# Kernel optimization log

Hardware: AMD Instinct MI355X
Metric: run time of the kernel (lower is better)

Reference implementation:

```python
import jax, jax.numpy as jnp
import numpy as np

B, N, D = 4, 1024, 512
H, Dv, Dq = 8, 64, 64
NUM_BUCKETS = 64
LN_EPS = 1e-5


def setup_inputs() -> dict:
    key = jax.random.key(0)
    ks = jax.random.split(key, 10)
    x = jax.random.normal(ks[0], (B, N, D), dtype=jnp.float32)
    ts = jnp.sort(jax.random.randint(ks[1], (B, N), 0, 1_000_000), axis=1).astype(jnp.int64)
    cm = jnp.triu(jnp.ones((N, N), dtype=bool), k=1)  # causal: mask j > i
    pm = jnp.zeros((B, N), dtype=bool)                # no padding
    uvqk = 0.02 * jax.random.normal(ks[2], (D, 2 * H * Dv + 2 * H * Dq), dtype=jnp.float32)
    lim = float(np.sqrt(6.0 / (H * Dv + D)))
    o_w = jax.random.uniform(ks[3], (H * Dv, D), minval=-lim, maxval=lim, dtype=jnp.float32)
    o_b = jnp.zeros((D,), dtype=jnp.float32)
    ln_x_w = jnp.ones((D,), jnp.float32); ln_x_b = jnp.zeros((D,), jnp.float32)
    ln_a_w = jnp.ones((H * Dv,), jnp.float32); ln_a_b = jnp.zeros((H * Dv,), jnp.float32)
    ts_w = 0.02 * jax.random.normal(ks[4], (NUM_BUCKETS + 1,), dtype=jnp.float32)
    pos_w = 0.02 * jax.random.normal(ks[5], (2 * N - 1,), dtype=jnp.float32)
    return {"x": x, "ts": ts, "cm": cm, "pm": pm, "uvqk": uvqk, "o_w": o_w, "o_b": o_b,
            "ln_x_w": ln_x_w, "ln_x_b": ln_x_b, "ln_a_w": ln_a_w, "ln_a_b": ln_a_b,
            "ts_w": ts_w, "pos_w": pos_w}


def _layernorm(x, w, b):
    m = jnp.mean(x, axis=-1, keepdims=True)
    v = jnp.mean(jnp.square(x - m), axis=-1, keepdims=True)
    return (x - m) / jnp.sqrt(v + LN_EPS) * w + b


def _rel_bias(ts, ts_w, pos_w):
    # positional part: pb[i, j] = pos_w[j - i + N - 1], shape [N, N]
    idx = jnp.arange(N)
    pb = pos_w[idx[None, :] - idx[:, None] + N - 1]
    # bucketed time part
    ext = jnp.concatenate([ts, ts[:, N - 1:N]], axis=1)           # [B, N+1]
    diff = ext[:, 1:, None] - ext[:, None, :-1]                   # [B, N, N]
    logd = jnp.log(jnp.maximum(jnp.abs(diff), 1).astype(jnp.float32))
    bk = jnp.clip((logd / 0.301).astype(jnp.int32), 0, NUM_BUCKETS)
    return pb[None] + ts_w[bk]                                    # [B, N, N]


def reference(x, ts, cm, pm, uvqk, o_w, o_b, ln_x_w, ln_x_b, ln_a_w, ln_a_b, ts_w, pos_w):
    nx = _layernorm(x, ln_x_w, ln_x_b)                            # [B, N, D]
    out = jax.nn.silu(jnp.einsum('bnd,de->bne', nx, uvqk))        # [B, N, 2HDv+2HDq]
    u, v, q, k = jnp.split(out, [H * Dv, 2 * H * Dv, 2 * H * Dv + H * Dq], axis=-1)
    q = q.reshape(B, N, H, Dq)
    k = k.reshape(B, N, H, Dq)
    v = v.reshape(B, N, H, Dv)
    qk = jnp.einsum('bihd,bjhd->bhij', q, k) + _rel_bias(ts, ts_w, pos_w)[:, None]
    qk = jax.nn.silu(qk) / N
    qk = jnp.where(cm[None, None], 0.0, qk)          # causal mask
    qk = jnp.where(pm[:, None, None, :], 0.0, qk)    # padding mask on keys
    ao = jnp.einsum('bhij,bjhd->bihd', qk, v).reshape(B, N, H * Dv)
    ao = _layernorm(ao, ln_a_w, ln_a_b)
    u = u.reshape(B, N, H * Dv)
    y = (u * ao) @ o_w + o_b + x
    return jnp.where(pm[:, :, None], 0.0, y)
```

## Files before the change

kernel.cpp:

```cpp
#include <hip/hip_runtime.h>


typedef __attribute__((ext_vector_type(8))) short short8;
typedef __attribute__((ext_vector_type(4))) short bf4;
typedef __attribute__((ext_vector_type(4))) float floatx4;

#define MFMA_BF16 __builtin_amdgcn_mfma_f32_16x16x32_bf16

static __device__ __forceinline__ short f2bf(float f) {
  unsigned u = __builtin_bit_cast(unsigned, f);
  u = (u + 0x7fffu + ((u >> 16) & 1u)) >> 16;
  return (short)u;
}
static __device__ __forceinline__ float bf2f(short s) {
  unsigned u = ((unsigned)(unsigned short)s) << 16;
  return __builtin_bit_cast(float, u);
}
static __device__ __forceinline__ float silu_f(float x) {
  return x / (1.f + __expf(-x));
}
static __device__ __forceinline__ void gl_lds16(const void* g, void* l) {
  __builtin_amdgcn_global_load_lds(
      (const __attribute__((address_space(1))) unsigned int*)g,
      (__attribute__((address_space(3))) unsigned int*)l, 16, 0, 0);
}

__global__ __launch_bounds__(256) void cvt_t_kernel(const float* __restrict__ src,
                                                    short* __restrict__ dst,
                                                    int R, int C) {
  __shared__ float tile[32][33];
  const int t = threadIdx.x;
  const int bc = blockIdx.x * 32, br = blockIdx.y * 32;
  const int c = t & 31, r0 = t >> 5;
#pragma unroll
  for (int p = 0; p < 4; ++p) {
    int r = r0 + p * 8;
    tile[r][c] = src[(size_t)(br + r) * C + bc + c];
  }
  __syncthreads();
#pragma unroll
  for (int p = 0; p < 4; ++p) {
    int r = r0 + p * 8;
    dst[(size_t)(bc + r) * R + br + c] = f2bf(tile[c][r]);
  }
}

__global__ __launch_bounds__(256) void ln_x_kernel(const float* __restrict__ x,
                                                   const float* __restrict__ w_,
                                                   const float* __restrict__ b_,
                                                   short* __restrict__ out) {
  const int lane = threadIdx.x & 63;
  const int row = (blockIdx.x << 2) + (threadIdx.x >> 6);
  const int c0 = lane * 8;
  const float* xr = x + (size_t)row * 512;
  float v[8];
  *(float4*)&v[0] = *(const float4*)(xr + c0);
  *(float4*)&v[4] = *(const float4*)(xr + c0 + 4);
  float s = 0.f, sq = 0.f;
#pragma unroll
  for (int e = 0; e < 8; ++e) { s += v[e]; sq += v[e] * v[e]; }
#pragma unroll
  for (int off = 32; off > 0; off >>= 1) {
    s += __shfl_xor(s, off);
    sq += __shfl_xor(sq, off);
  }
  float m = s * (1.f / 512.f);
  float var = sq * (1.f / 512.f) - m * m;
  float rinv = rsqrtf(var + 1e-5f);
  float wv[8], bv[8];
  *(float4*)&wv[0] = *(const float4*)(w_ + c0);
  *(float4*)&wv[4] = *(const float4*)(w_ + c0 + 4);
  *(float4*)&bv[0] = *(const float4*)(b_ + c0);
  *(float4*)&bv[4] = *(const float4*)(b_ + c0 + 4);
  short8 o;
#pragma unroll
  for (int e = 0; e < 8; ++e) o[e] = f2bf((v[e] - m) * rinv * wv[e] + bv[e]);
  *(short8*)(out + (size_t)row * 512 + c0) = o;
}

__global__ __launch_bounds__(256) void bias_kernel(const int* __restrict__ ts,
                                                   const float* __restrict__ ts_w,
                                                   const float* __restrict__ pos_w,
                                                   short* __restrict__ bias) {
  const int b = blockIdx.x >> 10, i = blockIdx.x & 1023;
  int ie = i + 1; if (ie > 1023) ie = 1023;
  const int tse = ts[(b << 10) + ie];
  const int j0 = threadIdx.x * 4;
  int4 tj = *(const int4*)&ts[(b << 10) + j0];
  const int* tjp = (const int*)&tj;
  bf4 o;
#pragma unroll
  for (int e = 0; e < 4; ++e) {
    int dt = tse - tjp[e];
    float ad = fabsf((float)dt);
    if (ad < 1.f) ad = 1.f;
    int bkt = (int)(__logf(ad) * (1.f / 0.301f));
    if (bkt > 64) bkt = 64;
    o[e] = f2bf(pos_w[j0 + e - i + 1023] + ts_w[bkt]);
  }
  *(bf4*)&bias[((size_t)blockIdx.x << 10) + j0] = o;
}

__global__ __launch_bounds__(256) void gemm1_kernel(
    const short* __restrict__ A, const short* __restrict__ Bt,
    short* __restrict__ u_buf, short* __restrict__ vt_buf,
    short* __restrict__ q_buf, short* __restrict__ k_buf) {
  __shared__ __align__(16) short As[128 * 32];
  __shared__ __align__(16) short Bs[128 * 32];
  const int t = threadIdx.x;
  const int lane = t & 63, w = t >> 6;
  const int quad = lane >> 4, l15 = lane & 15;
  const int m0 = blockIdx.x * 128, n0 = blockIdx.y * 128;
  const int wm = (w & 1) * 64, wn = (w >> 1) * 64;
  const int lr = lane >> 2, lc = (lane & 3) * 8;
  floatx4 acc[4][4];
#pragma unroll
  for (int i = 0; i < 4; ++i)
#pragma unroll
    for (int j = 0; j < 4; ++j) acc[i][j] = (floatx4){0.f, 0.f, 0.f, 0.f};

  for (int k0 = 0; k0 < 512; k0 += 32) {
    __syncthreads();
#pragma unroll
    for (int p = 0; p < 2; ++p) {
      int ra = w * 32 + p * 16;
      gl_lds16(&A[(size_t)(m0 + ra + lr) * 512 + k0 + lc], &As[ra * 32]);
      gl_lds16(&Bt[(size_t)(n0 + ra + lr) * 512 + k0 + lc], &Bs[ra * 32]);
    }
    __syncthreads();
    short8 af[4], bfr[4];
#pragma unroll
    for (int mi = 0; mi < 4; ++mi) af[mi] = *(const short8*)&As[(wm + mi * 16 + l15) * 32 + quad * 8];
#pragma unroll
    for (int ni = 0; ni < 4; ++ni) bfr[ni] = *(const short8*)&Bs[(wn + ni * 16 + l15) * 32 + quad * 8];
#pragma unroll
    for (int mi = 0; mi < 4; ++mi)
#pragma unroll
      for (int ni = 0; ni < 4; ++ni)
        acc[mi][ni] = MFMA_BF16(af[mi], bfr[ni], acc[mi][ni], 0, 0, 0);
  }
  const int seg = n0 >> 9, cbase = n0 & 511;
  if (seg == 0) {
#pragma unroll
    for (int mi = 0; mi < 4; ++mi)
#pragma unroll
      for (int ni = 0; ni < 4; ++ni)
#pragma unroll
        for (int r = 0; r < 4; ++r) {
          int row = m0 + wm + mi * 16 + quad * 4 + r;
          int c = cbase + wn + ni * 16 + l15;
          u_buf[(size_t)row * 512 + c] = f2bf(silu_f(acc[mi][ni][r]));
        }
  } else if (seg == 1) {
#pragma unroll
    for (int mi = 0; mi < 4; ++mi)
#pragma unroll
      for (int ni = 0; ni < 4; ++ni) {
        int c = cbase + wn + ni * 16 + l15;
        int h = c >> 6, d = c & 63;
        int row0 = m0 + wm + mi * 16 + quad * 4;
        int b_ = row0 >> 10, nb = row0 & 1023;
        bf4 sv;
#pragma unroll
        for (int r = 0; r < 4; ++r) sv[r] = f2bf(silu_f(acc[mi][ni][r]));
        *(bf4*)&vt_buf[(((size_t)(b_ * 8 + h) * 64 + d) << 10) + nb] = sv;
      }
  } else {
    short* dst = (seg == 2) ? q_buf : k_buf;
#pragma unroll
    for (int mi = 0; mi < 4; ++mi)
#pragma unroll
      for (int ni = 0; ni < 4; ++ni)
#pragma unroll
        for (int r = 0; r < 4; ++r) {
          int row = m0 + wm + mi * 16 + quad * 4 + r;
          int c = cbase + wn + ni * 16 + l15;
          int b_ = row >> 10, nseq = row & 1023;
          size_t idx = ((((size_t)(b_ * 8 + (c >> 6))) << 10) + nseq) * 64 + (c & 63);
          dst[idx] = f2bf(silu_f(acc[mi][ni][r]));
        }
  }
}

__global__ __launch_bounds__(256) void attn_kernel(
    const short* __restrict__ q_buf, const short* __restrict__ k_buf,
    const short* __restrict__ vt_buf, const short* __restrict__ bias_buf,
    short* __restrict__ ao_part) {
  __shared__ __align__(16) short q_s[64][72];
  __shared__ __align__(16) short k_s[64][72];
  __shared__ __align__(16) short vt_s[64][72];
  __shared__ __align__(16) short p_s[64][72];
  __shared__ __align__(16) short bias_s[64][72];

  const int t = threadIdx.x;
  const int lane = t & 63, w = t >> 6;
  const int quad = lane >> 4, l15 = lane & 15;
  const int bh = blockIdx.x, pair = blockIdx.y, jh = blockIdx.z;
  const int b = bh >> 3, h = bh & 7;
  const short* qh = q_buf + (size_t)bh * 65536;
  const short* kh = k_buf + (size_t)bh * 65536;
  const short* vth = vt_buf + (size_t)bh * 65536;
  const int sr = t >> 2, sc = (t & 3) * 16;

#pragma unroll
  for (int half = 0; half < 2; ++half) {
    const int it = half ? (15 - pair) : pair;
    const int i0 = it * 64;
    __syncthreads();
    *(float4*)&q_s[sr][sc] = *(const float4*)&qh[(size_t)(i0 + sr) * 64 + sc];
    *(float4*)&q_s[sr][sc + 8] = *(const float4*)&qh[(size_t)(i0 + sr) * 64 + sc + 8];
    floatx4 ao0 = {0.f, 0.f, 0.f, 0.f}, ao1 = ao0, ao2 = ao0, ao3 = ao0;
    for (int jt = jh; jt <= it; jt += 2) {
      const int j0 = jt * 64;
      __syncthreads();
      *(float4*)&k_s[sr][sc] = *(const float4*)&kh[(size_t)(j0 + sr) * 64 + sc];
      *(float4*)&k_s[sr][sc + 8] = *(const float4*)&kh[(size_t)(j0 + sr) * 64 + sc + 8];
      *(float4*)&vt_s[sr][sc] = *(const float4*)&vth[(size_t)sr * 1024 + j0 + sc];
      *(float4*)&vt_s[sr][sc + 8] = *(const float4*)&vth[(size_t)sr * 1024 + j0 + sc + 8];
      const size_t brow = ((size_t)(b * 1024 + i0 + sr) << 10) + j0 + sc;
      *(float4*)&bias_s[sr][sc] = *(const float4*)&bias_buf[brow];
      *(float4*)&bias_s[sr][sc + 8] = *(const float4*)&bias_buf[brow + 8];
      __syncthreads();
      floatx4 s0 = {0.f, 0.f, 0.f, 0.f}, s1 = s0, s2 = s0, s3 = s0;
#pragma unroll
      for (int kk = 0; kk < 64; kk += 32) {
        short8 aq = *(const short8*)&q_s[w * 16 + l15][kk + quad * 8];
        s0 = MFMA_BF16(aq, *(const short8*)&k_s[0 + l15][kk + quad * 8], s0, 0, 0, 0);
        s1 = MFMA_BF16(aq, *(const short8*)&k_s[16 + l15][kk + quad * 8], s1, 0, 0, 0);
        s2 = MFMA_BF16(aq, *(const short8*)&k_s[32 + l15][kk + quad * 8], s2, 0, 0, 0);
        s3 = MFMA_BF16(aq, *(const short8*)&k_s[48 + l15][kk + quad * 8], s3, 0, 0, 0);
      }
      const bool diag = (jt == it);
      floatx4 sv[4] = {s0, s1, s2, s3};
#pragma unroll
      for (int ni = 0; ni < 4; ++ni) {
        int j_loc = ni * 16 + l15;
#pragma unroll
        for (int r2 = 0; r2 < 4; ++r2) {
          int i_loc = w * 16 + quad * 4 + r2;
          float xx = sv[ni][r2] + bf2f(bias_s[i_loc][j_loc]);
          float pv = silu_f(xx) * (1.f / 1024.f);
          if (diag && j_loc > i_loc) pv = 0.f;
          p_s[i_loc][j_loc] = f2bf(pv);
        }
      }
#pragma unroll
      for (int kk = 0; kk < 64; kk += 32) {
        short8 ap = *(const short8*)&p_s[w * 16 + l15][kk + quad * 8];
        ao0 = MFMA_BF16(ap, *(const short8*)&vt_s[0 + l15][kk + quad * 8], ao0, 0, 0, 0);
        ao1 = MFMA_BF16(ap, *(const short8*)&vt_s[16 + l15][kk + quad * 8], ao1, 0, 0, 0);
        ao2 = MFMA_BF16(ap, *(const short8*)&vt_s[32 + l15][kk + quad * 8], ao2, 0, 0, 0);
        ao3 = MFMA_BF16(ap, *(const short8*)&vt_s[48 + l15][kk + quad * 8], ao3, 0, 0, 0);
      }
    }
    floatx4 aov[4] = {ao0, ao1, ao2, ao3};
    short* aod = ao_part + (size_t)jh * 2097152;
#pragma unroll
    for (int ni = 0; ni < 4; ++ni)
#pragma unroll
      for (int r2 = 0; r2 < 4; ++r2) {
        int gi = i0 + w * 16 + quad * 4 + r2;
        int d = ni * 16 + l15;
        aod[((size_t)(b * 1024 + gi)) * 512 + h * 64 + d] = f2bf(aov[ni][r2]);
      }
  }
}

__global__ __launch_bounds__(256) void ln_mul_kernel(
    const short* __restrict__ ao_part, const short* __restrict__ u,
    const float* __restrict__ w_, const float* __restrict__ b_,
    short* __restrict__ g) {
  const int lane = threadIdx.x & 63;
  const int row = (blockIdx.x << 2) + (threadIdx.x >> 6);
  const int c0 = lane * 8;
  short8 a0 = *(const short8*)(ao_part + (size_t)row * 512 + c0);
  short8 a1 = *(const short8*)(ao_part + 2097152 + (size_t)row * 512 + c0);
  float v[8];
#pragma unroll
  for (int e = 0; e < 8; ++e) v[e] = bf2f(a0[e]) + bf2f(a1[e]);
  float s = 0.f, sq = 0.f;
#pragma unroll
  for (int e = 0; e < 8; ++e) { s += v[e]; sq += v[e] * v[e]; }
#pragma unroll
  for (int off = 32; off > 0; off >>= 1) {
    s += __shfl_xor(s, off);
    sq += __shfl_xor(sq, off);
  }
  float m = s * (1.f / 512.f);
  float var = sq * (1.f / 512.f) - m * m;
  float rinv = rsqrtf(var + 1e-5f);
  float wv[8], bv[8];
  *(float4*)&wv[0] = *(const float4*)(w_ + c0);
  *(float4*)&wv[4] = *(const float4*)(w_ + c0 + 4);
  *(float4*)&bv[0] = *(const float4*)(b_ + c0);
  *(float4*)&bv[4] = *(const float4*)(b_ + c0 + 4);
  short8 uv = *(const short8*)(u + (size_t)row * 512 + c0);
  short8 o;
#pragma unroll
  for (int e = 0; e < 8; ++e)
    o[e] = f2bf(bf2f(uv[e]) * ((v[e] - m) * rinv * wv[e] + bv[e]));
  *(short8*)(g + (size_t)row * 512 + c0) = o;
}

__global__ __launch_bounds__(256) void gemm2_kernel(
    const short* __restrict__ G, const short* __restrict__ Wt,
    const float* __restrict__ o_b, const float* __restrict__ x,
    float* __restrict__ out) {
  __shared__ __align__(16) short As[64 * 32];
  __shared__ __align__(16) short Bs[128 * 32];
  const int t = threadIdx.x;
  const int lane = t & 63, w = t >> 6;
  const int quad = lane >> 4, l15 = lane & 15;
  const int m0 = blockIdx.x * 64, n0 = blockIdx.y * 128;
  const int wn = w * 32;
  const int lr = lane >> 2, lc = (lane & 3) * 8;
  floatx4 acc[4][2];
#pragma unroll
  for (int i = 0; i < 4; ++i)
#pragma unroll
    for (int j = 0; j < 2; ++j) acc[i][j] = (floatx4){0.f, 0.f, 0.f, 0.f};

  for (int k0 = 0; k0 < 512; k0 += 32) {
    __syncthreads();
    {
      int ra = w * 16;
      gl_lds16(&G[(size_t)(m0 + ra + lr) * 512 + k0 + lc], &As[ra * 32]);
    }
#pragma unroll
    for (int p = 0; p < 2; ++p) {
      int rb = w * 32 + p * 16;
      gl_lds16(&Wt[(size_t)(n0 + rb + lr) * 512 + k0 + lc], &Bs[rb * 32]);
    }
    __syncthreads();
    short8 af[4], bfr[2];
#pragma unroll
    for (int mi = 0; mi < 4; ++mi) af[mi] = *(const short8*)&As[(mi * 16 + l15) * 32 + quad * 8];
#pragma unroll
    for (int ni = 0; ni < 2; ++ni) bfr[ni] = *(const short8*)&Bs[(wn + ni * 16 + l15) * 32 + quad * 8];
#pragma unroll
    for (int mi = 0; mi < 4; ++mi)
#pragma unroll
      for (int ni = 0; ni < 2; ++ni)
        acc[mi][ni] = MFMA_BF16(af[mi], bfr[ni], acc[mi][ni], 0, 0, 0);
  }
#pragma unroll
  for (int mi = 0; mi < 4; ++mi)
#pragma unroll
    for (int ni = 0; ni < 2; ++ni)
#pragma unroll
      for (int r = 0; r < 4; ++r) {
        int row = m0 + mi * 16 + quad * 4 + r;
        int c = n0 + wn + ni * 16 + l15;
        out[(size_t)row * 512 + c] = acc[mi][ni][r] + o_b[c] + x[(size_t)row * 512 + c];
      }
}

extern "C" void kernel_launch(void* const* d_in, const int* in_sizes, int n_in,
                              void* d_out, int out_size, void* d_ws, size_t ws_size,
                              hipStream_t stream) {
  const float* x = (const float*)d_in[0];
  const int* ts = (const int*)d_in[1];
  const float* uvqk = (const float*)d_in[4];
  const float* o_w = (const float*)d_in[5];
  const float* o_b = (const float*)d_in[6];
  const float* ln_x_w = (const float*)d_in[7];
  const float* ln_x_b = (const float*)d_in[8];
  const float* ln_a_w = (const float*)d_in[9];
  const float* ln_a_b = (const float*)d_in[10];
  const float* ts_w = (const float*)d_in[11];
  const float* pos_w = (const float*)d_in[12];
  float* out = (float*)d_out;

  char* ws = (char*)d_ws;
  short* nx = (short*)(ws + 0);
  short* uvqk_t = (short*)(ws + 4194304);
  short* o_wt = (short*)(ws + 6291456);
  short* u_buf = (short*)(ws + 6815744);
  short* q_buf = (short*)(ws + 11010048);
  short* k_buf = (short*)(ws + 15204352);
  short* vt_buf = (short*)(ws + 19398656);
  short* bias_buf = (short*)(ws + 23592960);
  short* ao_part = (short*)(ws + 31981568);
  short* g_buf = nx;

  hipLaunchKernelGGL(cvt_t_kernel, dim3(64, 16), dim3(256), 0, stream, uvqk, uvqk_t, 512, 2048);
  hipLaunchKernelGGL(cvt_t_kernel, dim3(16, 16), dim3(256), 0, stream, o_w, o_wt, 512, 512);
  hipLaunchKernelGGL(ln_x_kernel, dim3(1024), dim3(256), 0, stream, x, ln_x_w, ln_x_b, nx);
  hipLaunchKernelGGL(bias_kernel, dim3(4096), dim3(256), 0, stream, ts, ts_w, pos_w, bias_buf);
  hipLaunchKernelGGL(gemm1_kernel, dim3(32, 16), dim3(256), 0, stream, nx, uvqk_t, u_buf, vt_buf, q_buf, k_buf);
  hipLaunchKernelGGL(attn_kernel, dim3(32, 8, 2), dim3(256), 0, stream, q_buf, k_buf, vt_buf, bias_buf, ao_part);
  hipLaunchKernelGGL(ln_mul_kernel, dim3(1024), dim3(256), 0, stream, ao_part, u_buf, ln_a_w, ln_a_b, g_buf);
  hipLaunchKernelGGL(gemm2_kernel, dim3(64, 4), dim3(256), 0, stream, g_buf, o_wt, o_b, x, out);
}
```

Before: 163.2 us.

## Merge prep kernels, deepen GEMM K-step, and register-prefetch attention tiles

```diff
diff --git a/kernel.cpp b/kernel.cpp
--- a/kernel.cpp
+++ b/kernel.cpp
@@ -25,88 +25,94 @@
       (__attribute__((address_space(3))) unsigned int*)l, 16, 0, 0);
 }
 
-__global__ __launch_bounds__(256) void cvt_t_kernel(const float* __restrict__ src,
-                                                    short* __restrict__ dst,
-                                                    int R, int C) {
+__global__ __launch_bounds__(256) void prep_kernel(
+    const float* __restrict__ x, const int* __restrict__ ts,
+    const float* __restrict__ uvqk, const float* __restrict__ o_w,
+    const float* __restrict__ ln_x_w, const float* __restrict__ ln_x_b,
+    const float* __restrict__ ts_w, const float* __restrict__ pos_w,
+    short* __restrict__ nx, short* __restrict__ uvqk_t,
+    short* __restrict__ o_wt, short* __restrict__ bias) {
   __shared__ float tile[32][33];
+  const int id = blockIdx.x;
   const int t = threadIdx.x;
-  const int bc = blockIdx.x * 32, br = blockIdx.y * 32;
-  const int c = t & 31, r0 = t >> 5;
-#pragma unroll
-  for (int p = 0; p < 4; ++p) {
-    int r = r0 + p * 8;
-    tile[r][c] = src[(size_t)(br + r) * C + bc + c];
-  }
-  __syncthreads();
-#pragma unroll
-  for (int p = 0; p < 4; ++p) {
-    int r = r0 + p * 8;
-    dst[(size_t)(bc + r) * R + br + c] = f2bf(tile[c][r]);
-  }
-}
-
-__global__ __launch_bounds__(256) void ln_x_kernel(const float* __restrict__ x,
-                                                   const float* __restrict__ w_,
-                                                   const float* __restrict__ b_,
-                                                   short* __restrict__ out) {
-  const int lane = threadIdx.x & 63;
-  const int row = (blockIdx.x << 2) + (threadIdx.x >> 6);
-  const int c0 = lane * 8;
-  const float* xr = x + (size_t)row * 512;
-  float v[8];
-  *(float4*)&v[0] = *(const float4*)(xr + c0);
-  *(float4*)&v[4] = *(const float4*)(xr + c0 + 4);
-  float s = 0.f, sq = 0.f;
-#pragma unroll
-  for (int e = 0; e < 8; ++e) { s += v[e]; sq += v[e] * v[e]; }
-#pragma unroll
-  for (int off = 32; off > 0; off >>= 1) {
-    s += __shfl_xor(s, off);
-    sq += __shfl_xor(sq, off);
-  }
-  float m = s * (1.f / 512.f);
-  float var = sq * (1.f / 512.f) - m * m;
-  float rinv = rsqrtf(var + 1e-5f);
-  float wv[8], bv[8];
-  *(float4*)&wv[0] = *(const float4*)(w_ + c0);
-  *(float4*)&wv[4] = *(const float4*)(w_ + c0 + 4);
-  *(float4*)&bv[0] = *(const float4*)(b_ + c0);
-  *(float4*)&bv[4] = *(const float4*)(b_ + c0 + 4);
-  short8 o;
-#pragma unroll
-  for (int e = 0; e < 8; ++e) o[e] = f2bf((v[e] - m) * rinv * wv[e] + bv[e]);
-  *(short8*)(out + (size_t)row * 512 + c0) = o;
-}
-
-__global__ __launch_bounds__(256) void bias_kernel(const int* __restrict__ ts,
-                                                   const float* __restrict__ ts_w,
-                                                   const float* __restrict__ pos_w,
-                                                   short* __restrict__ bias) {
-  const int b = blockIdx.x >> 10, i = blockIdx.x & 1023;
-  int ie = i + 1; if (ie > 1023) ie = 1023;
-  const int tse = ts[(b << 10) + ie];
-  const int j0 = threadIdx.x * 4;
-  int4 tj = *(const int4*)&ts[(b << 10) + j0];
-  const int* tjp = (const int*)&tj;
-  bf4 o;
-#pragma unroll
-  for (int e = 0; e < 4; ++e) {
-    int dt = tse - tjp[e];
-    float ad = fabsf((float)dt);
-    if (ad < 1.f) ad = 1.f;
-    int bkt = (int)(__logf(ad) * (1.f / 0.301f));
-    if (bkt > 64) bkt = 64;
-    o[e] = f2bf(pos_w[j0 + e - i + 1023] + ts_w[bkt]);
-  }
-  *(bf4*)&bias[((size_t)blockIdx.x << 10) + j0] = o;
+  if (id < 4096) {
+    const int b = id >> 10, i = id & 1023;
+    int ie = i + 1; if (ie > 1023) ie = 1023;
+    const int tse = ts[(b << 10) + ie];
+    const int j0 = t * 4;
+    int4 tj = *(const int4*)&ts[(b << 10) + j0];
+    const int* tjp = (const int*)&tj;
+    bf4 o;
+#pragma unroll
+    for (int e = 0; e < 4; ++e) {
+      int dt = tse - tjp[e];
+      float ad = fabsf((float)dt);
+      if (ad < 1.f) ad = 1.f;
+      int bkt = (int)(__logf(ad) * (1.f / 0.301f));
+      if (bkt > 64) bkt = 64;
+      o[e] = f2bf(pos_w[j0 + e - i + 1023] + ts_w[bkt]);
+    }
+    *(bf4*)&bias[((size_t)id << 10) + j0] = o;
+  } else if (id < 5120) {
+    const int lane = t & 63;
+    const int row = ((id - 4096) << 2) + (t >> 6);
+    const int c0 = lane * 8;
+    const float* xr = x + (size_t)row * 512;
+    float v[8];
+    *(float4*)&v[0] = *(const float4*)(xr + c0);
+    *(float4*)&v[4] = *(const float4*)(xr + c0 + 4);
+    float s = 0.f, sq = 0.f;
+#pragma unroll
+    for (int e = 0; e < 8; ++e) { s += v[e]; sq += v[e] * v[e]; }
+#pragma unroll
+    for (int off = 32; off > 0; off >>= 1) {
+      s += __shfl_xor(s, off);
+      sq += __shfl_xor(sq, off);
+    }
+    float m = s * (1.f / 512.f);
+    float var = sq * (1.f / 512.f) - m * m;
+    float rinv = rsqrtf(var + 1e-5f);
+    float wv[8], bv[8];
+    *(float4*)&wv[0] = *(const float4*)(ln_x_w + c0);
+    *(float4*)&wv[4] = *(const float4*)(ln_x_w + c0 + 4);
+    *(float4*)&bv[0] = *(const float4*)(ln_x_b + c0);
+    *(float4*)&bv[4] = *(const float4*)(ln_x_b + c0 + 4);
+    short8 o;
+#pragma unroll
+    for (int e = 0; e < 8; ++e) o[e] = f2bf((v[e] - m) * rinv * wv[e] + bv[e]);
+    *(short8*)(nx + (size_t)row * 512 + c0) = o;
+  } else {
+    const float* src; short* dst; int R, C, bc, br;
+    if (id < 6144) {
+      int idm = id - 5120;
+      src = uvqk; dst = uvqk_t; R = 512; C = 2048;
+      bc = (idm & 63) * 32; br = (idm >> 6) * 32;
+    } else {
+      int idm = id - 6144;
+      src = o_w; dst = o_wt; R = 512; C = 512;
+      bc = (idm & 15) * 32; br = (idm >> 4) * 32;
+    }
+    const int c = t & 31, r0 = t >> 5;
+#pragma unroll
+    for (int p = 0; p < 4; ++p) {
+      int r = r0 + p * 8;
+      tile[r][c] = src[(size_t)(br + r) * C + bc + c];
+    }
+    __syncthreads();
+#pragma unroll
+    for (int p = 0; p < 4; ++p) {
+      int r = r0 + p * 8;
+      dst[(size_t)(bc + r) * R + br + c] = f2bf(tile[c][r]);
+    }
+  }
 }
 
 __global__ __launch_bounds__(256) void gemm1_kernel(
     const short* __restrict__ A, const short* __restrict__ Bt,
     short* __restrict__ u_buf, short* __restrict__ vt_buf,
     short* __restrict__ q_buf, short* __restrict__ k_buf) {
-  __shared__ __align__(16) short As[128 * 32];
-  __shared__ __align__(16) short Bs[128 * 32];
+  __shared__ __align__(16) short As[2][128 * 32];
+  __shared__ __align__(16) short Bs[2][128 * 32];
   const int t = threadIdx.x;
   const int lane = t & 63, w = t >> 6;
   const int quad = lane >> 4, l15 = lane & 15;
@@ -119,25 +125,30 @@
 #pragma unroll
     for (int j = 0; j < 4; ++j) acc[i][j] = (floatx4){0.f, 0.f, 0.f, 0.f};
 
-  for (int k0 = 0; k0 < 512; k0 += 32) {
-    __syncthreads();
-#pragma unroll
-    for (int p = 0; p < 2; ++p) {
-      int ra = w * 32 + p * 16;
-      gl_lds16(&A[(size_t)(m0 + ra + lr) * 512 + k0 + lc], &As[ra * 32]);
-      gl_lds16(&Bt[(size_t)(n0 + ra + lr) * 512 + k0 + lc], &Bs[ra * 32]);
-    }
-    __syncthreads();
-    short8 af[4], bfr[4];
-#pragma unroll
-    for (int mi = 0; mi < 4; ++mi) af[mi] = *(const short8*)&As[(wm + mi * 16 + l15) * 32 + quad * 8];
-#pragma unroll
-    for (int ni = 0; ni < 4; ++ni) bfr[ni] = *(const short8*)&Bs[(wn + ni * 16 + l15) * 32 + quad * 8];
-#pragma unroll
-    for (int mi = 0; mi < 4; ++mi)
-#pragma unroll
-      for (int ni = 0; ni < 4; ++ni)
-        acc[mi][ni] = MFMA_BF16(af[mi], bfr[ni], acc[mi][ni], 0, 0, 0);
+  for (int k0 = 0; k0 < 512; k0 += 64) {
+    __syncthreads();
+#pragma unroll
+    for (int c = 0; c < 2; ++c)
+#pragma unroll
+      for (int p = 0; p < 2; ++p) {
+        int ra = w * 32 + p * 16;
+        gl_lds16(&A[(size_t)(m0 + ra + lr) * 512 + k0 + c * 32 + lc], &As[c][ra * 32]);
+        gl_lds16(&Bt[(size_t)(n0 + ra + lr) * 512 + k0 + c * 32 + lc], &Bs[c][ra * 32]);
+      }
+    __syncthreads();
+#pragma unroll
+    for (int c = 0; c < 2; ++c) {
+      short8 af[4], bfr[4];
+#pragma unroll
+      for (int mi = 0; mi < 4; ++mi) af[mi] = *(const short8*)&As[c][(wm + mi * 16 + l15) * 32 + quad * 8];
+#pragma unroll
+      for (int ni = 0; ni < 4; ++ni) bfr[ni] = *(const short8*)&Bs[c][(wn + ni * 16 + l15) * 32 + quad * 8];
+#pragma unroll
+      for (int mi = 0; mi < 4; ++mi)
+#pragma unroll
+        for (int ni = 0; ni < 4; ++ni)
+          acc[mi][ni] = MFMA_BF16(af[mi], bfr[ni], acc[mi][ni], 0, 0, 0);
+    }
   }
   const int seg = n0 >> 9, cbase = n0 & 511;
   if (seg == 0) {
@@ -206,20 +217,43 @@
   for (int half = 0; half < 2; ++half) {
     const int it = half ? (15 - pair) : pair;
     const int i0 = it * 64;
-    __syncthreads();
-    *(float4*)&q_s[sr][sc] = *(const float4*)&qh[(size_t)(i0 + sr) * 64 + sc];
-    *(float4*)&q_s[sr][sc + 8] = *(const float4*)&qh[(size_t)(i0 + sr) * 64 + sc + 8];
+    float4 qr0 = *(const float4*)&qh[(size_t)(i0 + sr) * 64 + sc];
+    float4 qr1 = *(const float4*)&qh[(size_t)(i0 + sr) * 64 + sc + 8];
+    __syncthreads();
+    *(float4*)&q_s[sr][sc] = qr0;
+    *(float4*)&q_s[sr][sc + 8] = qr1;
+    float4 kr0, kr1, vr0, vr1, br0, br1;
+    if (jh <= it) {
+      int j0 = jh * 64;
+      kr0 = *(const float4*)&kh[(size_t)(j0 + sr) * 64 + sc];
+      kr1 = *(const float4*)&kh[(size_t)(j0 + sr) * 64 + sc + 8];
+      vr0 = *(const float4*)&vth[(size_t)sr * 1024 + j0 + sc];
+      vr1 = *(const float4*)&vth[(size_t)sr * 1024 + j0 + sc + 8];
+      size_t brow = ((size_t)(b * 1024 + i0 + sr) << 10) + j0 + sc;
+      br0 = *(const float4*)&bias_buf[brow];
+      br1 = *(const float4*)&bias_buf[brow + 8];
+    }
     floatx4 ao0 = {0.f, 0.f, 0.f, 0.f}, ao1 = ao0, ao2 = ao0, ao3 = ao0;
     for (int jt = jh; jt <= it; jt += 2) {
       const int j0 = jt * 64;
       __syncthreads();
-      *(float4*)&k_s[sr][sc] = *(const float4*)&kh[(size_t)(j0 + sr) * 64 + sc];
-      *(float4*)&k_s[sr][sc + 8] = *(const float4*)&kh[(size_t)(j0 + sr) * 64 + sc + 8];
-      *(float4*)&vt_s[sr][sc] = *(const float4*)&vth[(size_t)sr * 1024 + j0 + sc];
-      *(float4*)&vt_s[sr][sc + 8] = *(const float4*)&vth[(size_t)sr * 1024 + j0 + sc + 8];
-      const size_t brow = ((size_t)(b * 1024 + i0 + sr) << 10) + j0 + sc;
-      *(float4*)&bias_s[sr][sc] = *(const float4*)&bias_buf[brow];
-      *(float4*)&bias_s[sr][sc + 8] = *(const float4*)&bias_buf[brow + 8];
+      *(float4*)&k_s[sr][sc] = kr0;
+      *(float4*)&k_s[sr][sc + 8] = kr1;
+      *(float4*)&vt_s[sr][sc] = vr0;
+      *(float4*)&vt_s[sr][sc + 8] = vr1;
+      *(float4*)&bias_s[sr][sc] = br0;
+      *(float4*)&bias_s[sr][sc + 8] = br1;
+      {
+        int jn = (jt + 2 <= it) ? jt + 2 : jt;
+        int jn0 = jn * 64;
+        kr0 = *(const float4*)&kh[(size_t)(jn0 + sr) * 64 + sc];
+        kr1 = *(const float4*)&kh[(size_t)(jn0 + sr) * 64 + sc + 8];
+        vr0 = *(const float4*)&vth[(size_t)sr * 1024 + jn0 + sc];
+        vr1 = *(const float4*)&vth[(size_t)sr * 1024 + jn0 + sc + 8];
+        size_t brow = ((size_t)(b * 1024 + i0 + sr) << 10) + jn0 + sc;
+        br0 = *(const float4*)&bias_buf[brow];
+        br1 = *(const float4*)&bias_buf[brow + 8];
+      }
       __syncthreads();
       floatx4 s0 = {0.f, 0.f, 0.f, 0.f}, s1 = s0, s2 = s0, s3 = s0;
 #pragma unroll
@@ -306,8 +340,8 @@
     const short* __restrict__ G, const short* __restrict__ Wt,
     const float* __restrict__ o_b, const float* __restrict__ x,
     float* __restrict__ out) {
-  __shared__ __align__(16) short As[64 * 32];
-  __shared__ __align__(16) short Bs[128 * 32];
+  __shared__ __align__(16) short As[2][64 * 32];
+  __shared__ __align__(16) short Bs[2][128 * 32];
   const int t = threadIdx.x;
   const int lane = t & 63, w = t >> 6;
   const int quad = lane >> 4, l15 = lane & 15;
@@ -320,28 +354,32 @@
 #pragma unroll
     for (int j = 0; j < 2; ++j) acc[i][j] = (floatx4){0.f, 0.f, 0.f, 0.f};
 
-  for (int k0 = 0; k0 < 512; k0 += 32) {
-    __syncthreads();
-    {
+  for (int k0 = 0; k0 < 512; k0 += 64) {
+    __syncthreads();
+#pragma unroll
+    for (int c = 0; c < 2; ++c) {
       int ra = w * 16;
-      gl_lds16(&G[(size_t)(m0 + ra + lr) * 512 + k0 + lc], &As[ra * 32]);
-    }
-#pragma unroll
-    for (int p = 0; p < 2; ++p) {
-      int rb = w * 32 + p * 16;
-      gl_lds16(&Wt[(size_t)(n0 + rb + lr) * 512 + k0 + lc], &Bs[rb * 32]);
-    }
-    __syncthreads();
-    short8 af[4], bfr[2];
-#pragma unroll
-    for (int mi = 0; mi < 4; ++mi) af[mi] = *(const short8*)&As[(mi * 16 + l15) * 32 + quad * 8];
-#pragma unroll
-    for (int ni = 0; ni < 2; ++ni) bfr[ni] = *(const short8*)&Bs[(wn + ni * 16 + l15) * 32 + quad * 8];
-#pragma unroll
-    for (int mi = 0; mi < 4; ++mi)
-#pragma unroll
-      for (int ni = 0; ni < 2; ++ni)
-        acc[mi][ni] = MFMA_BF16(af[mi], bfr[ni], acc[mi][ni], 0, 0, 0);
+      gl_lds16(&G[(size_t)(m0 + ra + lr) * 512 + k0 + c * 32 + lc], &As[c][ra * 32]);
+#pragma unroll
+      for (int p = 0; p < 2; ++p) {
+        int rb = w * 32 + p * 16;
+        gl_lds16(&Wt[(size_t)(n0 + rb + lr) * 512 + k0 + c * 32 + lc], &Bs[c][rb * 32]);
+      }
+    }
+    __syncthreads();
+#pragma unroll
+    for (int c = 0; c < 2; ++c) {
+      short8 af[4], bfr[2];
+#pragma unroll
+      for (int mi = 0; mi < 4; ++mi) af[mi] = *(const short8*)&As[c][(mi * 16 + l15) * 32 + quad * 8];
+#pragma unroll
+      for (int ni = 0; ni < 2; ++ni) bfr[ni] = *(const short8*)&Bs[c][(wn + ni * 16 + l15) * 32 + quad * 8];
+#pragma unroll
+      for (int mi = 0; mi < 4; ++mi)
+#pragma unroll
+        for (int ni = 0; ni < 2; ++ni)
+          acc[mi][ni] = MFMA_BF16(af[mi], bfr[ni], acc[mi][ni], 0, 0, 0);
+    }
   }
 #pragma unroll
   for (int mi = 0; mi < 4; ++mi)
@@ -383,10 +421,9 @@
   short* ao_part = (short*)(ws + 31981568);
   short* g_buf = nx;
 
-  hipLaunchKernelGGL(cvt_t_kernel, dim3(64, 16), dim3(256), 0, stream, uvqk, uvqk_t, 512, 2048);
-  hipLaunchKernelGGL(cvt_t_kernel, dim3(16, 16), dim3(256), 0, stream, o_w, o_wt, 512, 512);
-  hipLaunchKernelGGL(ln_x_kernel, dim3(1024), dim3(256), 0, stream, x, ln_x_w, ln_x_b, nx);
-  hipLaunchKernelGGL(bias_kernel, dim3(4096), dim3(256), 0, stream, ts, ts_w, pos_w, bias_buf);
+  hipLaunchKernelGGL(prep_kernel, dim3(6400), dim3(256), 0, stream,
+                     x, ts, uvqk, o_w, ln_x_w, ln_x_b, ts_w, pos_w,
+                     nx, uvqk_t, o_wt, bias_buf);
   hipLaunchKernelGGL(gemm1_kernel, dim3(32, 16), dim3(256), 0, stream, nx, uvqk_t, u_buf, vt_buf, q_buf, k_buf);
   hipLaunchKernelGGL(attn_kernel, dim3(32, 8, 2), dim3(256), 0, stream, q_buf, k_buf, vt_buf, bias_buf, ao_part);
   hipLaunchKernelGGL(ln_mul_kernel, dim3(1024), dim3(256), 0, stream, ao_part, u_buf, ln_a_w, ln_a_b, g_buf);
```

New measurement: 146.9 us. 10.0% less time.
